# Kernel tuning notes

Measured on AMD Instinct MI355X. Metric: run time of the kernel, lower is better.

## Reference

```python
import jax, jax.numpy as jnp
import numpy as np

N, L, D = 64, 1024, 512
SPAN = 8
LI = L - 2            # inner length after stripping CLS and last token
S = LI // SPAN        # 127 spans per sample
OUT = 300
EPS = 1e-5


def setup_inputs() -> dict:
    key = jax.random.key(0)
    k1, k2, k3 = jax.random.split(key, 3)
    t1 = jax.random.normal(k1, (N, L, D), dtype=jnp.float32)
    # contiguous non-empty spans (start, end) into the inner sequence, same for each sample
    starts = np.arange(S, dtype=np.int64) * SPAN
    ends = starts + SPAN
    word_seq = jnp.asarray(np.broadcast_to(np.stack([starts, ends], -1), (N, S, 2)).copy())
    key_padding_mask = jnp.zeros((N, S), dtype=bool)
    w_lin = jax.random.normal(k2, (OUT, D), dtype=jnp.float32) * (1.0 / np.sqrt(D))
    b_lin = jax.random.normal(k3, (OUT,), dtype=jnp.float32) * 0.02
    gamma = jnp.ones((OUT,), dtype=jnp.float32)
    beta = jnp.zeros((OUT,), dtype=jnp.float32)
    return {"t1": t1, "word_seq": word_seq, "key_padding_mask": key_padding_mask,
            "w_lin": w_lin, "b_lin": b_lin, "gamma": gamma, "beta": beta}


def reference(t1, word_seq, key_padding_mask, w_lin, b_lin, gamma, beta):
    use = t1[:, 0]                      # (N, D) cls token
    inner = t1[:, 1:-1, :]              # (N, LI, D)
    li = inner.shape[1]
    # prefix sums -> span sums via one gather (replaces per-span mean kernels)
    prefix = jnp.concatenate([jnp.zeros_like(inner[:, :1]), jnp.cumsum(inner, axis=1)], axis=1)  # (N, LI+1, D)
    start = jnp.minimum(word_seq[..., 0], li - 1)   # (N, S)
    end = jnp.minimum(word_seq[..., 1], li)
    span_sum = (jnp.take_along_axis(prefix, end[..., None], axis=1)
                - jnp.take_along_axis(prefix, start[..., None], axis=1))  # (N, S, D)
    count = (end - start).astype(inner.dtype)[..., None]                   # (N, S, 1) all > 0
    means = span_sum / count
    # linear_ then LayerNorm
    h = jnp.einsum('nsd,od->nso', means, w_lin) + b_lin                    # (N, S, OUT)
    mu = jnp.mean(h, axis=-1, keepdims=True)
    var = jnp.mean(jnp.square(h - mu), axis=-1, keepdims=True)
    out = (h - mu) * jax.lax.rsqrt(var + EPS) * gamma + beta
    return (out, use)
```

## Files before the change

### kernel.cpp

```cpp
#include <hip/hip_runtime.h>
#include <hip/hip_bf16.h>
#include <stdint.h>

#define N_   64
#define L_   1024
#define D_   512
#define S_   127
#define OUT_ 300
#define NT_  20
#define OUTP (NT_*16)
#define EPS_ 1e-5f
#define M_TOTAL (N_*S_)
#define NBLK (M_TOTAL/16)
#define AST  520
#define HSTR 325
#define PACK_BLOCKS 80
#define COPY_BLOCKS 32

typedef __attribute__((ext_vector_type(4))) float  float4v;
typedef __attribute__((ext_vector_type(8))) __bf16 bf16x8;
typedef __attribute__((ext_vector_type(4))) __bf16 bf16x4;

__global__ void prep_kernel(const float* __restrict__ w, __bf16* __restrict__ wpk,
                            const float* __restrict__ t1, float* __restrict__ ouse) {
    if (blockIdx.x < PACK_BLOCKS) {
        int idx = blockIdx.x * 256 + threadIdx.x;
        int t    = idx >> 10;
        int kt   = (idx >> 7) & 7;
        int ks   = (idx >> 6) & 1;
        int quad = (idx >> 4) & 3;
        int l16  = idx & 15;
        int o  = t * 16 + l16;
        int k0 = kt * 64 + ks * 32 + quad * 8;
        bf16x8 v;
        if (o < OUT_) {
            float4v f0 = *(const float4v*)(w + o * D_ + k0);
            float4v f1 = *(const float4v*)(w + o * D_ + k0 + 4);
            v[0]=(__bf16)f0[0]; v[1]=(__bf16)f0[1]; v[2]=(__bf16)f0[2]; v[3]=(__bf16)f0[3];
            v[4]=(__bf16)f1[0]; v[5]=(__bf16)f1[1]; v[6]=(__bf16)f1[2]; v[7]=(__bf16)f1[3];
        } else {
            #pragma unroll
            for (int j = 0; j < 8; ++j) v[j] = (__bf16)0.0f;
        }
        *(bf16x8*)(wpk + (size_t)idx * 8) = v;
    } else {
        int idx = (blockIdx.x - PACK_BLOCKS) * 256 + threadIdx.x;
        int n = idx >> 7, dg = idx & 127;
        float4v v = *(const float4v*)(t1 + (size_t)n * L_ * D_ + dg * 4);
        *(float4v*)(ouse + n * D_ + dg * 4) = v;
    }
}

__global__ __launch_bounds__(256) void enc_fused(
    const float* __restrict__ t1, const int* __restrict__ wseq,
    const __bf16* __restrict__ wpk, const float* __restrict__ b_lin,
    const float* __restrict__ gamma, const float* __restrict__ beta,
    float* __restrict__ out)
{
    __shared__ __align__(16) char smem[16 * HSTR * 4];
    __bf16* Alds = (__bf16*)smem;
    float*  hlds = (float*)smem;

    const int tid  = threadIdx.x;
    const int blk  = blockIdx.x;
    const int lane = tid & 63;
    const int wave = tid >> 6;
    const int quad = lane >> 4;
    const int ln16 = lane & 15;

    {
        const int row = tid >> 4;
        const int kg  = tid & 15;
        const int m   = blk * 16 + row;
        const int st  = min(wseq[2 * m],     L_ - 3);
        const int en  = min(wseq[2 * m + 1], L_ - 2);
        const int cnt = en - st;
        const float inv_cnt = 1.0f / (float)cnt;
        const int nn = m / S_;
        const float* base = t1 + ((size_t)nn * L_ + 1 + st) * D_ + kg * 4;
        #pragma unroll
        for (int c = 0; c < 8; ++c) {
            const int k0 = c * 64;
            float4v s = {0.f, 0.f, 0.f, 0.f};
            if (cnt == 8) {
                #pragma unroll
                for (int j = 0; j < 8; ++j) s += *(const float4v*)(base + j * D_ + k0);
            } else {
                for (int j = 0; j < cnt; ++j) s += *(const float4v*)(base + j * D_ + k0);
            }
            s *= inv_cnt;
            bf16x4 a4;
            a4[0]=(__bf16)s[0]; a4[1]=(__bf16)s[1]; a4[2]=(__bf16)s[2]; a4[3]=(__bf16)s[3];
            *(bf16x4*)(Alds + row * AST + k0 + kg * 4) = a4;
        }
    }
    __syncthreads();

    float4v acc[5];
    #pragma unroll
    for (int i = 0; i < 5; ++i) acc[i] = float4v{0.f, 0.f, 0.f, 0.f};
    const int t0 = wave * 5;

    #pragma unroll 2
    for (int kt = 0; kt < 8; ++kt) {
        bf16x8 af0 = *(const bf16x8*)(Alds + ln16 * AST + kt * 64 + quad * 8);
        bf16x8 af1 = *(const bf16x8*)(Alds + ln16 * AST + kt * 64 + 32 + quad * 8);
        const __bf16* bp = wpk + ((size_t)kt * 128 + lane) * 8;
        #pragma unroll
        for (int i = 0; i < 5; ++i) {
            const __bf16* bt = bp + (size_t)(t0 + i) * 8192;
            bf16x8 b0 = *(const bf16x8*)(bt);
            acc[i] = __builtin_amdgcn_mfma_f32_16x16x32_bf16(af0, b0, acc[i], 0, 0, 0);
            bf16x8 b1 = *(const bf16x8*)(bt + 512);
            acc[i] = __builtin_amdgcn_mfma_f32_16x16x32_bf16(af1, b1, acc[i], 0, 0, 0);
        }
    }
    __syncthreads();

    #pragma unroll
    for (int i = 0; i < 5; ++i) {
        const int col = (t0 + i) * 16 + ln16;
        const float bl = (col < OUT_) ? b_lin[col] : 0.0f;
        #pragma unroll
        for (int r = 0; r < 4; ++r)
            hlds[(quad * 4 + r) * HSTR + col] = acc[i][r] + bl;
    }
    __syncthreads();

    const int r  = tid >> 4;
    const int c0 = tid & 15;
    float sum = 0.f, sq = 0.f;
    #pragma unroll
    for (int i = 0; i < 19; ++i) {
        int c = c0 + 16 * i;
        if (c < OUT_) { float v = hlds[r * HSTR + c]; sum += v; sq += v * v; }
    }
    #pragma unroll
    for (int off = 8; off > 0; off >>= 1) {
        sum += __shfl_xor(sum, off);
        sq  += __shfl_xor(sq,  off);
    }
    const float mu  = sum * (1.0f / OUT_);
    const float var = sq * (1.0f / OUT_) - mu * mu;
    const float rs  = rsqrtf(var + EPS_);
    float* orow = out + (size_t)(blk * 16 + r) * OUT_;
    #pragma unroll
    for (int i = 0; i < 19; ++i) {
        int c = c0 + 16 * i;
        if (c < OUT_) {
            float v = hlds[r * HSTR + c];
            orow[c] = (v - mu) * rs * gamma[c] + beta[c];
        }
    }
}

extern "C" void kernel_launch(void* const* d_in, const int* in_sizes, int n_in,
                              void* d_out, int out_size, void* d_ws, size_t ws_size,
                              hipStream_t stream) {
    const float* t1    = (const float*)d_in[0];
    const int*   wseq  = (const int*)d_in[1];
    const float* w_lin = (const float*)d_in[3];
    const float* b_lin = (const float*)d_in[4];
    const float* gamma = (const float*)d_in[5];
    const float* beta  = (const float*)d_in[6];
    float* out  = (float*)d_out;
    __bf16* wpk = (__bf16*)d_ws;

    prep_kernel<<<PACK_BLOCKS + COPY_BLOCKS, 256, 0, stream>>>(
        w_lin, wpk, t1, out + (size_t)M_TOTAL * OUT_);
    enc_fused<<<NBLK, 256, 0, stream>>>(t1, wseq, wpk, b_lin, gamma, beta, out);
}
```

Baseline: 213.3 us.

## Fuse weight packing and CLS copy into single GEMM+LayerNorm kernel

Removes the separate prep kernel. The fp32 weights are now read directly in the MFMA loop and converted to bf16 on the fly, with zero-masking for padded output columns. The CLS-token copy is folded into the first 32 blocks of the main kernel. This saves one kernel launch and the packed-weight round trip through memory. In exchange, every block re-reads fp32 weights at twice the bytes with less coalesced access, and pays extra conversion ALU work inside the inner loop.

```diff
diff --git a/kernel.cpp b/kernel.cpp
--- a/kernel.cpp
+++ b/kernel.cpp
@@ -8,52 +8,19 @@
 #define S_   127
 #define OUT_ 300
 #define NT_  20
-#define OUTP (NT_*16)
 #define EPS_ 1e-5f
 #define M_TOTAL (N_*S_)
 #define NBLK (M_TOTAL/16)
 #define AST  520
 #define HSTR 325
-#define PACK_BLOCKS 80
-#define COPY_BLOCKS 32
 
 typedef __attribute__((ext_vector_type(4))) float  float4v;
 typedef __attribute__((ext_vector_type(8))) __bf16 bf16x8;
 typedef __attribute__((ext_vector_type(4))) __bf16 bf16x4;
 
-__global__ void prep_kernel(const float* __restrict__ w, __bf16* __restrict__ wpk,
-                            const float* __restrict__ t1, float* __restrict__ ouse) {
-    if (blockIdx.x < PACK_BLOCKS) {
-        int idx = blockIdx.x * 256 + threadIdx.x;
-        int t    = idx >> 10;
-        int kt   = (idx >> 7) & 7;
-        int ks   = (idx >> 6) & 1;
-        int quad = (idx >> 4) & 3;
-        int l16  = idx & 15;
-        int o  = t * 16 + l16;
-        int k0 = kt * 64 + ks * 32 + quad * 8;
-        bf16x8 v;
-        if (o < OUT_) {
-            float4v f0 = *(const float4v*)(w + o * D_ + k0);
-            float4v f1 = *(const float4v*)(w + o * D_ + k0 + 4);
-            v[0]=(__bf16)f0[0]; v[1]=(__bf16)f0[1]; v[2]=(__bf16)f0[2]; v[3]=(__bf16)f0[3];
-            v[4]=(__bf16)f1[0]; v[5]=(__bf16)f1[1]; v[6]=(__bf16)f1[2]; v[7]=(__bf16)f1[3];
-        } else {
-            #pragma unroll
-            for (int j = 0; j < 8; ++j) v[j] = (__bf16)0.0f;
-        }
-        *(bf16x8*)(wpk + (size_t)idx * 8) = v;
-    } else {
-        int idx = (blockIdx.x - PACK_BLOCKS) * 256 + threadIdx.x;
-        int n = idx >> 7, dg = idx & 127;
-        float4v v = *(const float4v*)(t1 + (size_t)n * L_ * D_ + dg * 4);
-        *(float4v*)(ouse + n * D_ + dg * 4) = v;
-    }
-}
-
-__global__ __launch_bounds__(256) void enc_fused(
+__global__ __launch_bounds__(256) void enc_all(
     const float* __restrict__ t1, const int* __restrict__ wseq,
-    const __bf16* __restrict__ wpk, const float* __restrict__ b_lin,
+    const float* __restrict__ w_lin, const float* __restrict__ b_lin,
     const float* __restrict__ gamma, const float* __restrict__ beta,
     float* __restrict__ out)
 {
@@ -67,6 +34,13 @@
     const int wave = tid >> 6;
     const int quad = lane >> 4;
     const int ln16 = lane & 15;
+
+    if (blk < 32) {
+        int idx = blk * 256 + tid;
+        int n = idx >> 7, dg = idx & 127;
+        float4v v = *(const float4v*)(t1 + (size_t)n * L_ * D_ + dg * 4);
+        *(float4v*)(out + (size_t)M_TOTAL * OUT_ + n * D_ + dg * 4) = v;
+    }
 
     {
         const int row = tid >> 4;
@@ -101,17 +75,38 @@
     for (int i = 0; i < 5; ++i) acc[i] = float4v{0.f, 0.f, 0.f, 0.f};
     const int t0 = wave * 5;
 
+    const float* wbase[5];
+    float osc[5];
+    #pragma unroll
+    for (int i = 0; i < 5; ++i) {
+        int o = (t0 + i) * 16 + ln16;
+        osc[i]   = (o < OUT_) ? 1.0f : 0.0f;
+        wbase[i] = w_lin + (size_t)min(o, OUT_ - 1) * D_ + quad * 8;
+    }
+
     #pragma unroll 2
     for (int kt = 0; kt < 8; ++kt) {
         bf16x8 af0 = *(const bf16x8*)(Alds + ln16 * AST + kt * 64 + quad * 8);
         bf16x8 af1 = *(const bf16x8*)(Alds + ln16 * AST + kt * 64 + 32 + quad * 8);
-        const __bf16* bp = wpk + ((size_t)kt * 128 + lane) * 8;
         #pragma unroll
         for (int i = 0; i < 5; ++i) {
-            const __bf16* bt = bp + (size_t)(t0 + i) * 8192;
-            bf16x8 b0 = *(const bf16x8*)(bt);
+            const float* p = wbase[i] + kt * 64;
+            const float sc = osc[i];
+            float4v f0 = *(const float4v*)(p);
+            float4v f1 = *(const float4v*)(p + 4);
+            bf16x8 b0;
+            b0[0]=(__bf16)(f0[0]*sc); b0[1]=(__bf16)(f0[1]*sc);
+            b0[2]=(__bf16)(f0[2]*sc); b0[3]=(__bf16)(f0[3]*sc);
+            b0[4]=(__bf16)(f1[0]*sc); b0[5]=(__bf16)(f1[1]*sc);
+            b0[6]=(__bf16)(f1[2]*sc); b0[7]=(__bf16)(f1[3]*sc);
             acc[i] = __builtin_amdgcn_mfma_f32_16x16x32_bf16(af0, b0, acc[i], 0, 0, 0);
-            bf16x8 b1 = *(const bf16x8*)(bt + 512);
+            float4v g0 = *(const float4v*)(p + 32);
+            float4v g1 = *(const float4v*)(p + 36);
+            bf16x8 b1;
+            b1[0]=(__bf16)(g0[0]*sc); b1[1]=(__bf16)(g0[1]*sc);
+            b1[2]=(__bf16)(g0[2]*sc); b1[3]=(__bf16)(g0[3]*sc);
+            b1[4]=(__bf16)(g1[0]*sc); b1[5]=(__bf16)(g1[1]*sc);
+            b1[6]=(__bf16)(g1[2]*sc); b1[7]=(__bf16)(g1[3]*sc);
             acc[i] = __builtin_amdgcn_mfma_f32_16x16x32_bf16(af1, b1, acc[i], 0, 0, 0);
         }
     }
@@ -163,10 +158,7 @@
     const float* b_lin = (const float*)d_in[4];
     const float* gamma = (const float*)d_in[5];
     const float* beta  = (const float*)d_in[6];
-    float* out  = (float*)d_out;
-    __bf16* wpk = (__bf16*)d_ws;
+    float* out = (float*)d_out;
 
-    prep_kernel<<<PACK_BLOCKS + COPY_BLOCKS, 256, 0, stream>>>(
-        w_lin, wpk, t1, out + (size_t)M_TOTAL * OUT_);
-    enc_fused<<<NBLK, 256, 0, stream>>>(t1, wseq, wpk, b_lin, gamma, beta, out);
+    enc_all<<<NBLK, 256, 0, stream>>>(t1, wseq, w_lin, b_lin, gamma, beta, out);
 }
```

Measured after the change: 243.4 us. +14.1%, slower.

## Split span-mean pooling into a separate kernel and load GEMM A-fragments from global

Applied to the files above, without the earlier changes.

Span-mean pooling moves out of the fused kernel into the prep kernel, which now writes bf16 means to workspace with one thread per (span, 4-column group). The GEMM+LayerNorm kernel then loads its A fragments straight from global memory into registers, dropping the LDS staging and a barrier, and declares two blocks per CU in its launch bounds. The aim is more memory-level parallelism for the bandwidth-bound 128MB read of t1, since the old design used only 508 blocks that each serialized a heavy load phase. The cost is an extra global round trip for the means buffer of about 8MB, and the weight packing now runs in the same launch as the means work.

```diff
diff --git a/kernel.cpp b/kernel.cpp
--- a/kernel.cpp
+++ b/kernel.cpp
@@ -8,23 +8,52 @@
 #define S_   127
 #define OUT_ 300
 #define NT_  20
-#define OUTP (NT_*16)
 #define EPS_ 1e-5f
 #define M_TOTAL (N_*S_)
-#define NBLK (M_TOTAL/16)
-#define AST  520
+#define GBLK (M_TOTAL/16)
+#define MEANS_BLOCKS 4064
+#define USE_BLOCKS   32
+#define PACK_BLOCKS  80
 #define HSTR 325
-#define PACK_BLOCKS 80
-#define COPY_BLOCKS 32
+#define MEANS_OFF 524288
 
 typedef __attribute__((ext_vector_type(4))) float  float4v;
 typedef __attribute__((ext_vector_type(8))) __bf16 bf16x8;
 typedef __attribute__((ext_vector_type(4))) __bf16 bf16x4;
 
-__global__ void prep_kernel(const float* __restrict__ w, __bf16* __restrict__ wpk,
-                            const float* __restrict__ t1, float* __restrict__ ouse) {
-    if (blockIdx.x < PACK_BLOCKS) {
-        int idx = blockIdx.x * 256 + threadIdx.x;
+__global__ __launch_bounds__(256) void prep_means(
+    const float* __restrict__ t1, const int* __restrict__ wseq,
+    const float* __restrict__ w, __bf16* __restrict__ wpk,
+    __bf16* __restrict__ means, float* __restrict__ ouse)
+{
+    const int blk = blockIdx.x, tid = threadIdx.x;
+    if (blk < MEANS_BLOCKS) {
+        int idx = blk * 256 + tid;
+        int m  = idx >> 7;
+        int dg = idx & 127;
+        int st = min(wseq[2 * m],     L_ - 3);
+        int en = min(wseq[2 * m + 1], L_ - 2);
+        int cnt = en - st;
+        int n = m / S_;
+        const float* base = t1 + ((size_t)n * L_ + 1 + st) * D_ + dg * 4;
+        float4v s = {0.f, 0.f, 0.f, 0.f};
+        if (cnt == 8) {
+            #pragma unroll
+            for (int j = 0; j < 8; ++j) s += *(const float4v*)(base + j * D_);
+        } else {
+            for (int j = 0; j < cnt; ++j) s += *(const float4v*)(base + j * D_);
+        }
+        s *= (1.0f / (float)cnt);
+        bf16x4 a4;
+        a4[0]=(__bf16)s[0]; a4[1]=(__bf16)s[1]; a4[2]=(__bf16)s[2]; a4[3]=(__bf16)s[3];
+        *(bf16x4*)(means + (size_t)m * D_ + dg * 4) = a4;
+    } else if (blk < MEANS_BLOCKS + USE_BLOCKS) {
+        int idx = (blk - MEANS_BLOCKS) * 256 + tid;
+        int n = idx >> 7, dg = idx & 127;
+        float4v v = *(const float4v*)(t1 + (size_t)n * L_ * D_ + dg * 4);
+        *(float4v*)(ouse + n * D_ + dg * 4) = v;
+    } else {
+        int idx = (blk - MEANS_BLOCKS - USE_BLOCKS) * 256 + tid;
         int t    = idx >> 10;
         int kt   = (idx >> 7) & 7;
         int ks   = (idx >> 6) & 1;
@@ -43,23 +72,15 @@
             for (int j = 0; j < 8; ++j) v[j] = (__bf16)0.0f;
         }
         *(bf16x8*)(wpk + (size_t)idx * 8) = v;
-    } else {
-        int idx = (blockIdx.x - PACK_BLOCKS) * 256 + threadIdx.x;
-        int n = idx >> 7, dg = idx & 127;
-        float4v v = *(const float4v*)(t1 + (size_t)n * L_ * D_ + dg * 4);
-        *(float4v*)(ouse + n * D_ + dg * 4) = v;
     }
 }
 
-__global__ __launch_bounds__(256) void enc_fused(
-    const float* __restrict__ t1, const int* __restrict__ wseq,
-    const __bf16* __restrict__ wpk, const float* __restrict__ b_lin,
-    const float* __restrict__ gamma, const float* __restrict__ beta,
-    float* __restrict__ out)
+__global__ __launch_bounds__(256, 2) void gemm_ln(
+    const __bf16* __restrict__ means, const __bf16* __restrict__ wpk,
+    const float* __restrict__ b_lin, const float* __restrict__ gamma,
+    const float* __restrict__ beta, float* __restrict__ out)
 {
-    __shared__ __align__(16) char smem[16 * HSTR * 4];
-    __bf16* Alds = (__bf16*)smem;
-    float*  hlds = (float*)smem;
+    __shared__ __align__(16) float hlds[16 * HSTR];
 
     const int tid  = threadIdx.x;
     const int blk  = blockIdx.x;
@@ -67,55 +88,33 @@
     const int wave = tid >> 6;
     const int quad = lane >> 4;
     const int ln16 = lane & 15;
+    const int m0   = blk * 16;
 
-    {
-        const int row = tid >> 4;
-        const int kg  = tid & 15;
-        const int m   = blk * 16 + row;
-        const int st  = min(wseq[2 * m],     L_ - 3);
-        const int en  = min(wseq[2 * m + 1], L_ - 2);
-        const int cnt = en - st;
-        const float inv_cnt = 1.0f / (float)cnt;
-        const int nn = m / S_;
-        const float* base = t1 + ((size_t)nn * L_ + 1 + st) * D_ + kg * 4;
-        #pragma unroll
-        for (int c = 0; c < 8; ++c) {
-            const int k0 = c * 64;
-            float4v s = {0.f, 0.f, 0.f, 0.f};
-            if (cnt == 8) {
-                #pragma unroll
-                for (int j = 0; j < 8; ++j) s += *(const float4v*)(base + j * D_ + k0);
-            } else {
-                for (int j = 0; j < cnt; ++j) s += *(const float4v*)(base + j * D_ + k0);
-            }
-            s *= inv_cnt;
-            bf16x4 a4;
-            a4[0]=(__bf16)s[0]; a4[1]=(__bf16)s[1]; a4[2]=(__bf16)s[2]; a4[3]=(__bf16)s[3];
-            *(bf16x4*)(Alds + row * AST + k0 + kg * 4) = a4;
-        }
+    const __bf16* ab = means + (size_t)(m0 + ln16) * D_ + quad * 8;
+    bf16x8 A0[8], A1[8];
+    #pragma unroll
+    for (int kt = 0; kt < 8; ++kt) {
+        A0[kt] = *(const bf16x8*)(ab + kt * 64);
+        A1[kt] = *(const bf16x8*)(ab + kt * 64 + 32);
     }
-    __syncthreads();
 
     float4v acc[5];
     #pragma unroll
     for (int i = 0; i < 5; ++i) acc[i] = float4v{0.f, 0.f, 0.f, 0.f};
     const int t0 = wave * 5;
 
-    #pragma unroll 2
+    #pragma unroll
     for (int kt = 0; kt < 8; ++kt) {
-        bf16x8 af0 = *(const bf16x8*)(Alds + ln16 * AST + kt * 64 + quad * 8);
-        bf16x8 af1 = *(const bf16x8*)(Alds + ln16 * AST + kt * 64 + 32 + quad * 8);
         const __bf16* bp = wpk + ((size_t)kt * 128 + lane) * 8;
         #pragma unroll
         for (int i = 0; i < 5; ++i) {
             const __bf16* bt = bp + (size_t)(t0 + i) * 8192;
             bf16x8 b0 = *(const bf16x8*)(bt);
-            acc[i] = __builtin_amdgcn_mfma_f32_16x16x32_bf16(af0, b0, acc[i], 0, 0, 0);
             bf16x8 b1 = *(const bf16x8*)(bt + 512);
-            acc[i] = __builtin_amdgcn_mfma_f32_16x16x32_bf16(af1, b1, acc[i], 0, 0, 0);
+            acc[i] = __builtin_amdgcn_mfma_f32_16x16x32_bf16(A0[kt], b0, acc[i], 0, 0, 0);
+            acc[i] = __builtin_amdgcn_mfma_f32_16x16x32_bf16(A1[kt], b1, acc[i], 0, 0, 0);
         }
     }
-    __syncthreads();
 
     #pragma unroll
     for (int i = 0; i < 5; ++i) {
@@ -143,7 +142,7 @@
     const float mu  = sum * (1.0f / OUT_);
     const float var = sq * (1.0f / OUT_) - mu * mu;
     const float rs  = rsqrtf(var + EPS_);
-    float* orow = out + (size_t)(blk * 16 + r) * OUT_;
+    float* orow = out + (size_t)(m0 + r) * OUT_;
     #pragma unroll
     for (int i = 0; i < 19; ++i) {
         int c = c0 + 16 * i;
@@ -164,9 +163,10 @@
     const float* gamma = (const float*)d_in[5];
     const float* beta  = (const float*)d_in[6];
     float* out  = (float*)d_out;
-    __bf16* wpk = (__bf16*)d_ws;
+    __bf16* wpk   = (__bf16*)d_ws;
+    __bf16* means = (__bf16*)((char*)d_ws + MEANS_OFF);
 
-    prep_kernel<<<PACK_BLOCKS + COPY_BLOCKS, 256, 0, stream>>>(
-        w_lin, wpk, t1, out + (size_t)M_TOTAL * OUT_);
-    enc_fused<<<NBLK, 256, 0, stream>>>(t1, wseq, wpk, b_lin, gamma, beta, out);
+    prep_means<<<MEANS_BLOCKS + USE_BLOCKS + PACK_BLOCKS, 256, 0, stream>>>(
+        t1, wseq, w_lin, wpk, means, out + (size_t)M_TOTAL * OUT_);
+    gemm_ln<<<GBLK, 256, 0, stream>>>(means, wpk, b_lin, gamma, beta, out);
 }
```

New measurement: 215.4 us. Within noise of the previous version (+1.0%).
